# Kernel tuning notes

Hardware: AMD Instinct MI355X
Metric: run time of the kernel (lower is better)

The kernel has to match this reference:

```python
import jax, jax.numpy as jnp
import numpy as np

LN_EPS = 1e-5

def setup_inputs() -> dict:
    key = jax.random.key(0)
    ks = jax.random.split(key, 10)
    N, E, H, V, L, OUT, G = 100000, 600000, 128, 65, 4, 32, 64
    x_tokens = jax.random.randint(ks[0], (N, 2), 0, V, dtype=jnp.int32)
    edge_index = jax.random.randint(ks[1], (2, E), 0, N, dtype=jnp.int32)
    batch = jnp.sort(jax.random.randint(ks[2], (N,), 0, G)).astype(jnp.int64)
    s = 0.05
    key_emb = jax.random.normal(ks[3], (V, H), jnp.float32) * s
    val_emb = jax.random.normal(ks[4], (V, H), jnp.float32) * s
    Ws = jax.random.normal(ks[5], (L, H, H), jnp.float32) * (1.0 / np.sqrt(H))
    bs = jax.random.normal(ks[6], (L, H), jnp.float32) * s
    ln_g = jnp.ones((L, H), jnp.float32)
    ln_b = jnp.zeros((L, H), jnp.float32)
    out_W = jax.random.normal(ks[7], (OUT, H), jnp.float32) * (1.0 / np.sqrt(H))
    return {"x_tokens": x_tokens, "edge_index": edge_index, "batch": batch,
            "key_emb": key_emb, "val_emb": val_emb, "Ws": Ws, "bs": bs,
            "ln_g": ln_g, "ln_b": ln_b, "out_W": out_W}

def _layer_norm(x, g, b):
    mu = jnp.mean(x, axis=-1, keepdims=True)
    var = jnp.mean(jnp.square(x - mu), axis=-1, keepdims=True)
    return (x - mu) * jax.lax.rsqrt(var + LN_EPS) * g + b

def reference(x_tokens, edge_index, batch, key_emb, val_emb, Ws, bs, ln_g, ln_b, out_W):
    N = x_tokens.shape[0]
    L = Ws.shape[0]
    # layer-0: key + value embedding lookup -> [N, H]
    x = key_emb[x_tokens[:, 0]] + val_emb[x_tokens[:, 1]]
    # GCN normalization with self-loops (computed once; edges fixed per layer)
    loop = jnp.arange(N, dtype=edge_index.dtype)
    src = jnp.concatenate([edge_index[0], loop])  # [E+N]
    dst = jnp.concatenate([edge_index[1], loop])
    deg = jax.ops.segment_sum(jnp.ones_like(dst, dtype=x.dtype), dst, num_segments=N)
    dis = jnp.where(deg > 0, jax.lax.rsqrt(jnp.maximum(deg, 1.0)), 0.0)
    norm = (dis[src] * dis[dst])[:, None]  # [E+N, 1]
    for i in range(L):
        xw = x @ Ws[i]  # [N, H]
        agg = jax.ops.segment_sum(norm * xw[src], dst, num_segments=N) + bs[i]
        new_x = jax.nn.relu(agg)          # use_activation
        x = x + new_x                      # use_residual
        x = _layer_norm(x, ln_g[i], ln_b[i])  # use_layer_norm
    logits = x @ out_W.T  # Linear(bias=False) -> [N, out_dim]
    return logits
```

## Files before the change

### kernel.cpp

```cpp
#include <hip/hip_runtime.h>

#define H 128
#define LN_EPS 1e-5f
#define TROW 66

typedef unsigned short u16;
typedef unsigned int u32;
typedef __attribute__((ext_vector_type(8))) short bf16x8;
typedef __attribute__((ext_vector_type(4))) float f32x4;

__device__ __forceinline__ float bflo(u32 u){ return __uint_as_float(u << 16); }
__device__ __forceinline__ float bfhi(u32 u){ return __uint_as_float(u & 0xFFFF0000u); }
__device__ __forceinline__ float bf1(u16 u){ return __uint_as_float(((u32)u) << 16); }
__device__ __forceinline__ u16 f2bu(float f){
  u32 u = __float_as_uint(f);
  return (u16)((u + 0x7FFFu + ((u >> 16) & 1u)) >> 16);
}

__device__ __forceinline__ float ldf(const void* p, int i, bool isbf){
  return isbf ? bf1(reinterpret_cast<const u16*>(p)[i])
              : reinterpret_cast<const float*>(p)[i];
}


__global__ void k_convert(const void* __restrict__ kemb, const void* __restrict__ vemb,
                          const void* __restrict__ Ws,   const void* __restrict__ bs,
                          const void* __restrict__ lng,  const void* __restrict__ lnb,
                          const void* __restrict__ outW,
                          float* __restrict__ kemb_f, float* __restrict__ vemb_f,
                          u16* __restrict__ W_c, float* __restrict__ bs_f,
                          float* __restrict__ lng_f, float* __restrict__ lnb_f,
                          u16* __restrict__ outW_b, int* __restrict__ flag,
                          int V, int L, int OUT){
  bool isbf = (*reinterpret_cast<const u32*>(lng) == 0x3F803F80u);
  if (blockIdx.x == 0 && threadIdx.x == 0) flag[0] = isbf ? 1 : 0;
  int i = blockIdx.x * blockDim.x + threadIdx.x;
  int nEmb = V * H;
  int nW   = L * H * H;
  int nVec = L * H;
  int nOut = OUT * H;
  if (i < nEmb){ kemb_f[i] = ldf(kemb, i, isbf); vemb_f[i] = ldf(vemb, i, isbf); }
  if (i < nW){
    int j = i & 7, lane = (i >> 3) & 63, g = i >> 9;
    int s = g & 3, cg = (g >> 2) & 7, l = g >> 5;
    int k = s * 32 + (lane >> 4) * 8 + j;
    int n = cg * 16 + (lane & 15);
    W_c[i] = f2bu(ldf(Ws, l * H * H + k * H + n, isbf));
  }
  if (i < nVec){ bs_f[i] = ldf(bs, i, isbf); lng_f[i] = ldf(lng, i, isbf);
                 lnb_f[i] = ldf(lnb, i, isbf); }
  if (i < nOut){ outW_b[i] = f2bu(ldf(outW, i, isbf)); }
}


__global__ void k_count(const int* __restrict__ dst, int E, int* __restrict__ deg){
  int i = blockIdx.x * blockDim.x + threadIdx.x;
  if (i < E) atomicAdd(&deg[dst[i]], 1);
}

__device__ __forceinline__ int paddedLen(int d){ return (d + 4) & ~3; }

__global__ void k_bsum(const int* __restrict__ deg, int* __restrict__ bsum, int N){
  __shared__ int sh[256];
  int i = blockIdx.x * 256 + threadIdx.x;
  sh[threadIdx.x] = (i < N) ? paddedLen(deg[i]) : 0;
  __syncthreads();
  for (int off = 128; off > 0; off >>= 1){
    if (threadIdx.x < off) sh[threadIdx.x] += sh[threadIdx.x + off];
    __syncthreads();
  }
  if (threadIdx.x == 0) bsum[blockIdx.x] = sh[0];
}

__global__ void k_bscan(int* __restrict__ bsum, int nb){
  __shared__ int sh[1024];
  int t = threadIdx.x;
  sh[t] = (t < nb) ? bsum[t] : 0;
  __syncthreads();
  for (int off = 1; off < 1024; off <<= 1){
    int add = (t >= off) ? sh[t - off] : 0;
    __syncthreads();
    sh[t] += add;
    __syncthreads();
  }
  if (t < nb) bsum[t] = (t > 0) ? sh[t - 1] : 0;
}

__global__ void k_scan2(const int* __restrict__ deg, const int* __restrict__ bsum,
                        int* __restrict__ row_ptr, float* __restrict__ dis,
                        int* __restrict__ cursor, int2* __restrict__ csr, int N){
  __shared__ int sh[256];
  int i = blockIdx.x * 256 + threadIdx.x;
  int d = (i < N) ? deg[i] : 0;
  int v = (i < N) ? paddedLen(d) : 0;
  sh[threadIdx.x] = v;
  __syncthreads();
  for (int off = 1; off < 256; off <<= 1){
    int add = (threadIdx.x >= off) ? sh[threadIdx.x - off] : 0;
    __syncthreads();
    sh[threadIdx.x] += add;
    __syncthreads();
  }
  int excl = sh[threadIdx.x] - v + bsum[blockIdx.x];
  if (i < N){
    row_ptr[i] = excl;
    float r = rsqrtf((float)(d + 1));
    dis[i] = r;
    cursor[i] = 1;
    csr[excl] = make_int2(i * (H / 2), __float_as_int(r * r));
    for (int p = excl + d + 1; p < excl + v; p++)
      csr[p] = make_int2(0, 0);
  }
  if (i == N - 1) row_ptr[N] = excl + v;
}

__global__ void k_fill(const int* __restrict__ src, const int* __restrict__ dst, int E,
                       const float* __restrict__ dis, const int* __restrict__ row_ptr,
                       int* __restrict__ cursor, int2* __restrict__ csr){
  int i = blockIdx.x * blockDim.x + threadIdx.x;
  if (i >= E) return;
  int s = src[i], d = dst[i];
  int pos = atomicAdd(&cursor[d], 1);
  csr[row_ptr[d] + pos] = make_int2(s * (H / 2), __float_as_int(dis[s] * dis[d]));
}


__global__ __launch_bounds__(256) void k_embed(const int* __restrict__ tok,
                        const float* __restrict__ kemb, const float* __restrict__ vemb,
                        u16* __restrict__ xb, int N){
  int n = blockIdx.x * 4 + (threadIdx.x >> 6);
  if (n >= N) return;
  int h0 = (threadIdx.x & 63) * 2;
  int t0 = tok[n * 2], t1 = tok[n * 2 + 1];
  float2 k2 = *reinterpret_cast<const float2*>(&kemb[t0 * H + h0]);
  float2 v2 = *reinterpret_cast<const float2*>(&vemb[t1 * H + h0]);
  *reinterpret_cast<u32*>(&xb[(size_t)n * H + h0]) =
      (u32)f2bu(k2.x + v2.x) | ((u32)f2bu(k2.y + v2.y) << 16);
}


__global__ __launch_bounds__(256) void k_gemm(const u16* __restrict__ xb,
                                              const u16* __restrict__ Wc,
                                              u16* __restrict__ xw, int npairs){
  int wid = threadIdx.x >> 6, lane = threadIdx.x & 63;
  int sp = wid >> 1;
  int ch = wid & 1;
  int r = lane & 15, kq = lane >> 4;
  bf16x8 wf[4][4];
  #pragma unroll
  for (int c = 0; c < 4; c++)
    #pragma unroll
    for (int s = 0; s < 4; s++)
      wf[c][s] = *reinterpret_cast<const bf16x8*>(
          Wc + (size_t)((((ch * 4 + c) * 4 + s) * 64 + lane) << 3));
  for (int p = blockIdx.x; p < npairs; p += gridDim.x){
    int node0 = (p * 2 + sp) << 4;
    const u16* xrow = xb + (size_t)node0 * H + r * H + kq * 8;
    bf16x8 xf[4];
    #pragma unroll
    for (int s = 0; s < 4; s++)
      xf[s] = *reinterpret_cast<const bf16x8*>(xrow + s * 32);
    f32x4 acc[4] = {{0,0,0,0},{0,0,0,0},{0,0,0,0},{0,0,0,0}};
    #pragma unroll
    for (int s = 0; s < 4; s++)
      #pragma unroll
      for (int c = 0; c < 4; c++)
        acc[c] = __builtin_amdgcn_mfma_f32_16x16x32_bf16(wf[c][s], xf[s], acc[c], 0, 0, 0);
    u16* orow = xw + (size_t)(node0 + r) * H + ch * 64 + kq * 4;
    #pragma unroll
    for (int c = 0; c < 4; c++){
      u32 lo = (u32)f2bu(acc[c][0]) | ((u32)f2bu(acc[c][1]) << 16);
      u32 hi = (u32)f2bu(acc[c][2]) | ((u32)f2bu(acc[c][3]) << 16);
      *reinterpret_cast<uint2*>(orow + c * 16) = make_uint2(lo, hi);
    }
  }
}


__device__ __forceinline__ void gather4(const u32* __restrict__ xw32,
    const int* __restrict__ row_ptr, const int2* __restrict__ csr,
    const float* __restrict__ bias, const float* __restrict__ gamma,
    const float* __restrict__ beta,
    u16* __restrict__ xb, int N, u32* __restrict__ tile, bool writeGlobal){
  int lane = threadIdx.x & 63;
  int w = threadIdx.x >> 6;
  int n0 = blockIdx.x * 16 + 4 * w;
  int h0 = lane * 2;
  const int4* csr4 = reinterpret_cast<const int4*>(csr);
  int rp0 = __builtin_amdgcn_readfirstlane(row_ptr[min(n0, N)]);
  int rp1 = __builtin_amdgcn_readfirstlane(row_ptr[min(n0 + 1, N)]);
  int rp2 = __builtin_amdgcn_readfirstlane(row_ptr[min(n0 + 2, N)]);
  int rp3 = __builtin_amdgcn_readfirstlane(row_ptr[min(n0 + 3, N)]);
  int rp4 = __builtin_amdgcn_readfirstlane(row_ptr[min(n0 + 4, N)]);
  int l0 = rp1 - rp0, l1 = rp2 - rp1, l2 = rp3 - rp2, l3 = rp4 - rp3;
  bool val0 = n0 < N, val1 = n0 + 1 < N, val2 = n0 + 2 < N, val3 = n0 + 3 < N;
  u32 xv0 = val0 ? *reinterpret_cast<const u32*>(&xb[(size_t)n0 * H + h0]) : 0u;
  u32 xv1 = val1 ? *reinterpret_cast<const u32*>(&xb[(size_t)(n0 + 1) * H + h0]) : 0u;
  u32 xv2 = val2 ? *reinterpret_cast<const u32*>(&xb[(size_t)(n0 + 2) * H + h0]) : 0u;
  u32 xv3 = val3 ? *reinterpret_cast<const u32*>(&xb[(size_t)(n0 + 3) * H + h0]) : 0u;
  float2 b2 = *reinterpret_cast<const float2*>(&bias[h0]);
  float2 g2 = *reinterpret_cast<const float2*>(&gamma[h0]);
  float2 t2 = *reinterpret_cast<const float2*>(&beta[h0]);
  float a00 = 0.f, a01 = 0.f, a10 = 0.f, a11 = 0.f;
  float a20 = 0.f, a21 = 0.f, a30 = 0.f, a31 = 0.f;
#define EDGE(CX, CY, A0, A1) { \
    u32 cx = (u32)__builtin_amdgcn_readfirstlane(CX); \
    float wgt = __uint_as_float((u32)__builtin_amdgcn_readfirstlane(CY)); \
    u32 v = xw32[cx + lane]; \
    A0 = fmaf(wgt, bflo(v), A0); A1 = fmaf(wgt, bfhi(v), A1); }
  int c01 = min(l0, l1), c23 = min(l2, l3), c4 = min(c01, c23);
  int i = 0;
  for (; i < c4; i += 4){
    int4 A0 = csr4[(rp0 + i) >> 1], B0 = csr4[((rp0 + i) >> 1) + 1];
    int4 A1 = csr4[(rp1 + i) >> 1], B1 = csr4[((rp1 + i) >> 1) + 1];
    int4 A2 = csr4[(rp2 + i) >> 1], B2 = csr4[((rp2 + i) >> 1) + 1];
    int4 A3 = csr4[(rp3 + i) >> 1], B3 = csr4[((rp3 + i) >> 1) + 1];
    EDGE(A0.x, A0.y, a00, a01) EDGE(A1.x, A1.y, a10, a11)
    EDGE(A2.x, A2.y, a20, a21) EDGE(A3.x, A3.y, a30, a31)
    EDGE(A0.z, A0.w, a00, a01) EDGE(A1.z, A1.w, a10, a11)
    EDGE(A2.z, A2.w, a20, a21) EDGE(A3.z, A3.w, a30, a31)
    EDGE(B0.x, B0.y, a00, a01) EDGE(B1.x, B1.y, a10, a11)
    EDGE(B2.x, B2.y, a20, a21) EDGE(B3.x, B3.y, a30, a31)
    EDGE(B0.z, B0.w, a00, a01) EDGE(B1.z, B1.w, a10, a11)
    EDGE(B2.z, B2.w, a20, a21) EDGE(B3.z, B3.w, a30, a31)
  }
  int j = i;
  for (; j < c01; j += 4){
    int4 A0 = csr4[(rp0 + j) >> 1], B0 = csr4[((rp0 + j) >> 1) + 1];
    int4 A1 = csr4[(rp1 + j) >> 1], B1 = csr4[((rp1 + j) >> 1) + 1];
    EDGE(A0.x, A0.y, a00, a01) EDGE(A1.x, A1.y, a10, a11)
    EDGE(A0.z, A0.w, a00, a01) EDGE(A1.z, A1.w, a10, a11)
    EDGE(B0.x, B0.y, a00, a01) EDGE(B1.x, B1.y, a10, a11)
    EDGE(B0.z, B0.w, a00, a01) EDGE(B1.z, B1.w, a10, a11)
  }
  int j0 = j;
  for (; j0 < l0; j0 += 4){
    int4 A0 = csr4[(rp0 + j0) >> 1], B0 = csr4[((rp0 + j0) >> 1) + 1];
    EDGE(A0.x, A0.y, a00, a01) EDGE(A0.z, A0.w, a00, a01)
    EDGE(B0.x, B0.y, a00, a01) EDGE(B0.z, B0.w, a00, a01)
  }
  int j1 = j;
  for (; j1 < l1; j1 += 4){
    int4 A1 = csr4[(rp1 + j1) >> 1], B1 = csr4[((rp1 + j1) >> 1) + 1];
    EDGE(A1.x, A1.y, a10, a11) EDGE(A1.z, A1.w, a10, a11)
    EDGE(B1.x, B1.y, a10, a11) EDGE(B1.z, B1.w, a10, a11)
  }
  int k = i;
  for (; k < c23; k += 4){
    int4 A2 = csr4[(rp2 + k) >> 1], B2 = csr4[((rp2 + k) >> 1) + 1];
    int4 A3 = csr4[(rp3 + k) >> 1], B3 = csr4[((rp3 + k) >> 1) + 1];
    EDGE(A2.x, A2.y, a20, a21) EDGE(A3.x, A3.y, a30, a31)
    EDGE(A2.z, A2.w, a20, a21) EDGE(A3.z, A3.w, a30, a31)
    EDGE(B2.x, B2.y, a20, a21) EDGE(B3.x, B3.y, a30, a31)
    EDGE(B2.z, B2.w, a20, a21) EDGE(B3.z, B3.w, a30, a31)
  }
  int k2 = k;
  for (; k2 < l2; k2 += 4){
    int4 A2 = csr4[(rp2 + k2) >> 1], B2 = csr4[((rp2 + k2) >> 1) + 1];
    EDGE(A2.x, A2.y, a20, a21) EDGE(A2.z, A2.w, a20, a21)
    EDGE(B2.x, B2.y, a20, a21) EDGE(B2.z, B2.w, a20, a21)
  }
  int k3 = k;
  for (; k3 < l3; k3 += 4){
    int4 A3 = csr4[(rp3 + k3) >> 1], B3 = csr4[((rp3 + k3) >> 1) + 1];
    EDGE(A3.x, A3.y, a30, a31) EDGE(A3.z, A3.w, a30, a31)
    EDGE(B3.x, B3.y, a30, a31) EDGE(B3.z, B3.w, a30, a31)
  }
#undef EDGE
  float v0 = fmaxf(a00 + b2.x, 0.f) + bflo(xv0), v1 = fmaxf(a01 + b2.y, 0.f) + bfhi(xv0);
  float u0 = fmaxf(a10 + b2.x, 0.f) + bflo(xv1), u1 = fmaxf(a11 + b2.y, 0.f) + bfhi(xv1);
  float p0 = fmaxf(a20 + b2.x, 0.f) + bflo(xv2), p1 = fmaxf(a21 + b2.y, 0.f) + bfhi(xv2);
  float r0 = fmaxf(a30 + b2.x, 0.f) + bflo(xv3), r1 = fmaxf(a31 + b2.y, 0.f) + bfhi(xv3);
  float s0 = v0 + v1, s1 = u0 + u1, s2 = p0 + p1, s3 = r0 + r1;
  #pragma unroll
  for (int off = 32; off > 0; off >>= 1){
    s0 += __shfl_xor(s0, off); s1 += __shfl_xor(s1, off);
    s2 += __shfl_xor(s2, off); s3 += __shfl_xor(s3, off);
  }
  float mu0 = s0 * (1.f / 128.f), mu1 = s1 * (1.f / 128.f);
  float mu2 = s2 * (1.f / 128.f), mu3 = s3 * (1.f / 128.f);
  float d00 = v0 - mu0, d01 = v1 - mu0, d10 = u0 - mu1, d11 = u1 - mu1;
  float d20 = p0 - mu2, d21 = p1 - mu2, d30 = r0 - mu3, d31 = r1 - mu3;
  float q0 = d00 * d00 + d01 * d01, q1 = d10 * d10 + d11 * d11;
  float q2 = d20 * d20 + d21 * d21, q3 = d30 * d30 + d31 * d31;
  #pragma unroll
  for (int off = 32; off > 0; off >>= 1){
    q0 += __shfl_xor(q0, off); q1 += __shfl_xor(q1, off);
    q2 += __shfl_xor(q2, off); q3 += __shfl_xor(q3, off);
  }
  float i0 = rsqrtf(q0 * (1.f / 128.f) + LN_EPS), i1 = rsqrtf(q1 * (1.f / 128.f) + LN_EPS);
  float i2 = rsqrtf(q2 * (1.f / 128.f) + LN_EPS), i3 = rsqrtf(q3 * (1.f / 128.f) + LN_EPS);
  u32 w0 = (u32)f2bu(d00 * i0 * g2.x + t2.x) | ((u32)f2bu(d01 * i0 * g2.y + t2.y) << 16);
  u32 w1 = (u32)f2bu(d10 * i1 * g2.x + t2.x) | ((u32)f2bu(d11 * i1 * g2.y + t2.y) << 16);
  u32 w2 = (u32)f2bu(d20 * i2 * g2.x + t2.x) | ((u32)f2bu(d21 * i2 * g2.y + t2.y) << 16);
  u32 w3 = (u32)f2bu(d30 * i3 * g2.x + t2.x) | ((u32)f2bu(d31 * i3 * g2.y + t2.y) << 16);
  tile[(4 * w + 0) * TROW + lane] = val0 ? w0 : 0u;
  tile[(4 * w + 1) * TROW + lane] = val1 ? w1 : 0u;
  tile[(4 * w + 2) * TROW + lane] = val2 ? w2 : 0u;
  tile[(4 * w + 3) * TROW + lane] = val3 ? w3 : 0u;
  if (writeGlobal){
    if (val0) *reinterpret_cast<u32*>(&xb[(size_t)n0 * H + h0]) = w0;
    if (val1) *reinterpret_cast<u32*>(&xb[(size_t)(n0 + 1) * H + h0]) = w1;
    if (val2) *reinterpret_cast<u32*>(&xb[(size_t)(n0 + 2) * H + h0]) = w2;
    if (val3) *reinterpret_cast<u32*>(&xb[(size_t)(n0 + 3) * H + h0]) = w3;
  }
}

__global__ __launch_bounds__(256) void k_fgemm(const u32* __restrict__ xw32,
    const int* __restrict__ row_ptr, const int2* __restrict__ csr,
    const float* __restrict__ bias, const float* __restrict__ gamma,
    const float* __restrict__ beta,
    u16* __restrict__ xb, const u16* __restrict__ Wc,
    u16* __restrict__ xw_out, int N){
  __shared__ u32 tile[16 * TROW];
  int lane = threadIdx.x & 63, w = threadIdx.x >> 6;
  int r = lane & 15, kq = lane >> 4;
  bf16x8 wfr[2][4];
  #pragma unroll
  for (int c = 0; c < 2; c++)
    #pragma unroll
    for (int s = 0; s < 4; s++)
      wfr[c][s] = *reinterpret_cast<const bf16x8*>(
          Wc + (size_t)((((2 * w + c) * 4 + s) * 64 + lane) << 3));
  gather4(xw32, row_ptr, csr, bias, gamma, beta, xb, N, tile, true);
  __syncthreads();
  int node = blockIdx.x * 16 + r;
  if (node >= N) return;
  const u16* t16 = reinterpret_cast<const u16*>(tile);
  f32x4 acc[2] = {{0,0,0,0},{0,0,0,0}};
  #pragma unroll
  for (int s = 0; s < 4; s++){
    bf16x8 xf = *reinterpret_cast<const bf16x8*>(t16 + r * (2 * TROW) + s * 32 + kq * 8);
    #pragma unroll
    for (int c = 0; c < 2; c++)
      acc[c] = __builtin_amdgcn_mfma_f32_16x16x32_bf16(wfr[c][s], xf, acc[c], 0, 0, 0);
  }
  #pragma unroll
  for (int c = 0; c < 2; c++){
    u32 lo = (u32)f2bu(acc[c][0]) | ((u32)f2bu(acc[c][1]) << 16);
    u32 hi = (u32)f2bu(acc[c][2]) | ((u32)f2bu(acc[c][3]) << 16);
    *reinterpret_cast<uint2*>(xw_out + (size_t)node * H + (2 * w + c) * 16 + kq * 4) =
        make_uint2(lo, hi);
  }
}

__global__ __launch_bounds__(256) void k_fout(const u32* __restrict__ xw32,
    const int* __restrict__ row_ptr, const int2* __restrict__ csr,
    const float* __restrict__ bias, const float* __restrict__ gamma,
    const float* __restrict__ beta,
    u16* __restrict__ xb, const u16* __restrict__ oWb,
    u16* __restrict__ out16, float* __restrict__ outf,
    const int* __restrict__ flag, int N){
  __shared__ u32 tile[16 * TROW];
  int lane = threadIdx.x & 63, w = threadIdx.x >> 6;
  int r = lane & 15, kq = lane >> 4;
  bf16x8 wfr[4];
  if (w < 2){
    #pragma unroll
    for (int s = 0; s < 4; s++)
      wfr[s] = *reinterpret_cast<const bf16x8*>(oWb + (w * 16 + r) * H + s * 32 + kq * 8);
  }
  gather4(xw32, row_ptr, csr, bias, gamma, beta, xb, N, tile, false);
  __syncthreads();
  if (w >= 2) return;
  int node = blockIdx.x * 16 + r;
  if (node >= N) return;
  const u16* t16 = reinterpret_cast<const u16*>(tile);
  f32x4 acc = {0.f, 0.f, 0.f, 0.f};
  #pragma unroll
  for (int s = 0; s < 4; s++){
    bf16x8 xf = *reinterpret_cast<const bf16x8*>(t16 + r * (2 * TROW) + s * 32 + kq * 8);
    acc = __builtin_amdgcn_mfma_f32_16x16x32_bf16(wfr[s], xf, acc, 0, 0, 0);
  }
  if (flag[0]){
    u32 lo = (u32)f2bu(acc[0]) | ((u32)f2bu(acc[1]) << 16);
    u32 hi = (u32)f2bu(acc[2]) | ((u32)f2bu(acc[3]) << 16);
    *reinterpret_cast<uint2*>(out16 + (size_t)node * 32 + w * 16 + kq * 4) =
        make_uint2(lo, hi);
  } else {
    *reinterpret_cast<f32x4*>(outf + (size_t)node * 32 + w * 16 + kq * 4) = acc;
  }
}


extern "C" void kernel_launch(void* const* d_in, const int* in_sizes, int n_in,
                              void* d_out, int out_size, void* d_ws, size_t ws_size,
                              hipStream_t stream){
  const int*  x_tokens = (const int*)d_in[0];
  const int*  edge_idx = (const int*)d_in[1];
  const void* kemb = d_in[3];
  const void* vemb = d_in[4];
  const void* Ws   = d_in[5];
  const void* bs   = d_in[6];
  const void* lng  = d_in[7];
  const void* lnb  = d_in[8];
  const void* outW = d_in[9];

  int N   = in_sizes[0] / 2;
  int E   = in_sizes[1] / 2;
  int V   = in_sizes[3] / H;
  int L   = in_sizes[5] / (H * H);
  int OUT = in_sizes[9] / H;

  char* ws = (char*)d_ws;
  size_t off = 0;
  auto alloc = [&](size_t bytes) -> void* {
    void* p = ws + off;
    off += (bytes + 255) & ~(size_t)255;
    return p;
  };
  u16*   xb     = (u16*)  alloc((size_t)N * H * 2);
  u16*   xwA    = (u16*)  alloc((size_t)N * H * 2);
  u16*   xwB    = (u16*)  alloc((size_t)N * H * 2);
  int*   deg    = (int*)  alloc((size_t)N * 4);
  int*   cursor = (int*)  alloc((size_t)N * 4);
  int*   row_ptr= (int*)  alloc((size_t)(N + 1) * 4);
  float* dis    = (float*)alloc((size_t)N * 4);
  int*   bsum   = (int*)  alloc(1024 * 4);
  int2*  csr    = (int2*) alloc(((size_t)E + 4 * (size_t)N) * 8);
  float* kemb_f = (float*)alloc((size_t)V * H * 4);
  float* vemb_f = (float*)alloc((size_t)V * H * 4);
  u16*   W_c    = (u16*)  alloc((size_t)L * H * H * 2);
  float* bs_f   = (float*)alloc((size_t)L * H * 4);
  float* lng_f  = (float*)alloc((size_t)L * H * 4);
  float* lnb_f  = (float*)alloc((size_t)L * H * 4);
  u16*   outW_b = (u16*)  alloc((size_t)OUT * H * 2);
  int*   flag   = (int*)  alloc(256);

  const int* esrc = edge_idx;
  const int* edst = edge_idx + E;

  (void)hipMemsetAsync(deg, 0, (size_t)N * 4, stream);

  int convTotal = L * H * H;
  int cb = (convTotal + 255) / 256;
  k_convert<<<cb, 256, 0, stream>>>(kemb, vemb, Ws, bs, lng, lnb, outW,
                                    kemb_f, vemb_f, W_c, bs_f, lng_f, lnb_f,
                                    outW_b, flag, V, L, OUT);

  int eb = (E + 255) / 256;
  int nb = (N + 255) / 256;
  k_count<<<eb, 256, 0, stream>>>(edst, E, deg);
  k_bsum <<<nb, 256, 0, stream>>>(deg, bsum, N);
  k_bscan<<<1, 1024, 0, stream>>>(bsum, nb);
  k_scan2<<<nb, 256, 0, stream>>>(deg, bsum, row_ptr, dis, cursor, csr, N);
  k_fill <<<eb, 256, 0, stream>>>(esrc, edst, E, dis, row_ptr, cursor, csr);
  k_embed<<<(N + 3) / 4, 256, 0, stream>>>(x_tokens, kemb_f, vemb_f, xb, N);

  int nstrips = (N + 15) / 16;
  int npairs  = (nstrips + 1) / 2;
  k_gemm<<<1024, 256, 0, stream>>>(xb, W_c, xwA, npairs);
  u16* xw_in = xwA; u16* xw_out = xwB;
  for (int l = 0; l < L - 1; l++){
    k_fgemm<<<nstrips, 256, 0, stream>>>((const u32*)xw_in, row_ptr, csr,
                                         bs_f + l * H, lng_f + l * H, lnb_f + l * H,
                                         xb, W_c + (size_t)(l + 1) * H * H,
                                         xw_out, N);
    u16* t = xw_in; xw_in = xw_out; xw_out = t;
  }
  k_fout<<<nstrips, 256, 0, stream>>>((const u32*)xw_in, row_ptr, csr,
                                      bs_f + (L - 1) * H, lng_f + (L - 1) * H,
                                      lnb_f + (L - 1) * H,
                                      xb, outW_b, (u16*)d_out, (float*)d_out,
                                      flag, N);
}
```

Before: 284.5 us.

## Sort nodes by degree so each wave processes similar-length rows

Adds a degree histogram, scan and counting-sort permutation so fused gather/GEMM kernels handle nodes in descending-degree order. Each wave of four nodes then has closely matched edge counts, which cuts the tail loops and divergence where one long row stalls the other three. The cost is three extra small kernels, one more level of indirection per node, and scattered rather than contiguous reads and writes of xb and outputs.

Result: slower. 1.028 ms (+261.4%).

```diff
diff --git a/kernel.cpp b/kernel.cpp
--- a/kernel.cpp
+++ b/kernel.cpp
@@ -125,6 +125,35 @@
 }
 
 
+__global__ void k_hist(const int* __restrict__ deg, int* __restrict__ hist, int N){
+  int i = blockIdx.x * blockDim.x + threadIdx.x;
+  if (i < N) atomicAdd(&hist[min(deg[i], 255)], 1);
+}
+
+__global__ void k_hscan(const int* __restrict__ hist, int* __restrict__ bcur, int N){
+  __shared__ int sh[256];
+  int t = threadIdx.x;
+  sh[t] = hist[t];
+  __syncthreads();
+  for (int off = 1; off < 256; off <<= 1){
+    int add = (t >= off) ? sh[t - off] : 0;
+    __syncthreads();
+    sh[t] += add;
+    __syncthreads();
+  }
+  bcur[t] = N - sh[t];
+}
+
+__global__ void k_perm(const int* __restrict__ deg, int* __restrict__ bcur,
+                       int* __restrict__ perm, int N){
+  int i = blockIdx.x * blockDim.x + threadIdx.x;
+  if (i >= N) return;
+  int b = min(deg[i], 255);
+  int pos = atomicAdd(&bcur[b], 1);
+  perm[pos] = i;
+}
+
+
 __global__ __launch_bounds__(256) void k_embed(const int* __restrict__ tok,
                         const float* __restrict__ kemb, const float* __restrict__ vemb,
                         u16* __restrict__ xb, int N){
@@ -179,6 +208,7 @@
 
 __device__ __forceinline__ void gather4(const u32* __restrict__ xw32,
     const int* __restrict__ row_ptr, const int2* __restrict__ csr,
+    const int* __restrict__ perm,
     const float* __restrict__ bias, const float* __restrict__ gamma,
     const float* __restrict__ beta,
     u16* __restrict__ xb, int N, u32* __restrict__ tile, bool writeGlobal){
@@ -187,17 +217,23 @@
   int n0 = blockIdx.x * 16 + 4 * w;
   int h0 = lane * 2;
   const int4* csr4 = reinterpret_cast<const int4*>(csr);
-  int rp0 = __builtin_amdgcn_readfirstlane(row_ptr[min(n0, N)]);
-  int rp1 = __builtin_amdgcn_readfirstlane(row_ptr[min(n0 + 1, N)]);
-  int rp2 = __builtin_amdgcn_readfirstlane(row_ptr[min(n0 + 2, N)]);
-  int rp3 = __builtin_amdgcn_readfirstlane(row_ptr[min(n0 + 3, N)]);
-  int rp4 = __builtin_amdgcn_readfirstlane(row_ptr[min(n0 + 4, N)]);
-  int l0 = rp1 - rp0, l1 = rp2 - rp1, l2 = rp3 - rp2, l3 = rp4 - rp3;
   bool val0 = n0 < N, val1 = n0 + 1 < N, val2 = n0 + 2 < N, val3 = n0 + 3 < N;
-  u32 xv0 = val0 ? *reinterpret_cast<const u32*>(&xb[(size_t)n0 * H + h0]) : 0u;
-  u32 xv1 = val1 ? *reinterpret_cast<const u32*>(&xb[(size_t)(n0 + 1) * H + h0]) : 0u;
-  u32 xv2 = val2 ? *reinterpret_cast<const u32*>(&xb[(size_t)(n0 + 2) * H + h0]) : 0u;
-  u32 xv3 = val3 ? *reinterpret_cast<const u32*>(&xb[(size_t)(n0 + 3) * H + h0]) : 0u;
+  int p0 = __builtin_amdgcn_readfirstlane(perm[min(n0,     N - 1)]);
+  int p1 = __builtin_amdgcn_readfirstlane(perm[min(n0 + 1, N - 1)]);
+  int p2 = __builtin_amdgcn_readfirstlane(perm[min(n0 + 2, N - 1)]);
+  int p3 = __builtin_amdgcn_readfirstlane(perm[min(n0 + 3, N - 1)]);
+  int rp0 = __builtin_amdgcn_readfirstlane(row_ptr[p0]);
+  int rp1 = __builtin_amdgcn_readfirstlane(row_ptr[p1]);
+  int rp2 = __builtin_amdgcn_readfirstlane(row_ptr[p2]);
+  int rp3 = __builtin_amdgcn_readfirstlane(row_ptr[p3]);
+  int l0 = val0 ? __builtin_amdgcn_readfirstlane(row_ptr[p0 + 1]) - rp0 : 0;
+  int l1 = val1 ? __builtin_amdgcn_readfirstlane(row_ptr[p1 + 1]) - rp1 : 0;
+  int l2 = val2 ? __builtin_amdgcn_readfirstlane(row_ptr[p2 + 1]) - rp2 : 0;
+  int l3 = val3 ? __builtin_amdgcn_readfirstlane(row_ptr[p3 + 1]) - rp3 : 0;
+  u32 xv0 = val0 ? *reinterpret_cast<const u32*>(&xb[(size_t)p0 * H + h0]) : 0u;
+  u32 xv1 = val1 ? *reinterpret_cast<const u32*>(&xb[(size_t)p1 * H + h0]) : 0u;
+  u32 xv2 = val2 ? *reinterpret_cast<const u32*>(&xb[(size_t)p2 * H + h0]) : 0u;
+  u32 xv3 = val3 ? *reinterpret_cast<const u32*>(&xb[(size_t)p3 * H + h0]) : 0u;
   float2 b2 = *reinterpret_cast<const float2*>(&bias[h0]);
   float2 g2 = *reinterpret_cast<const float2*>(&gamma[h0]);
   float2 t2 = *reinterpret_cast<const float2*>(&beta[h0]);
@@ -269,9 +305,9 @@
 #undef EDGE
   float v0 = fmaxf(a00 + b2.x, 0.f) + bflo(xv0), v1 = fmaxf(a01 + b2.y, 0.f) + bfhi(xv0);
   float u0 = fmaxf(a10 + b2.x, 0.f) + bflo(xv1), u1 = fmaxf(a11 + b2.y, 0.f) + bfhi(xv1);
-  float p0 = fmaxf(a20 + b2.x, 0.f) + bflo(xv2), p1 = fmaxf(a21 + b2.y, 0.f) + bfhi(xv2);
+  float p0f = fmaxf(a20 + b2.x, 0.f) + bflo(xv2), p1f = fmaxf(a21 + b2.y, 0.f) + bfhi(xv2);
   float r0 = fmaxf(a30 + b2.x, 0.f) + bflo(xv3), r1 = fmaxf(a31 + b2.y, 0.f) + bfhi(xv3);
-  float s0 = v0 + v1, s1 = u0 + u1, s2 = p0 + p1, s3 = r0 + r1;
+  float s0 = v0 + v1, s1 = u0 + u1, s2 = p0f + p1f, s3 = r0 + r1;
   #pragma unroll
   for (int off = 32; off > 0; off >>= 1){
     s0 += __shfl_xor(s0, off); s1 += __shfl_xor(s1, off);
@@ -280,7 +316,7 @@
   float mu0 = s0 * (1.f / 128.f), mu1 = s1 * (1.f / 128.f);
   float mu2 = s2 * (1.f / 128.f), mu3 = s3 * (1.f / 128.f);
   float d00 = v0 - mu0, d01 = v1 - mu0, d10 = u0 - mu1, d11 = u1 - mu1;
-  float d20 = p0 - mu2, d21 = p1 - mu2, d30 = r0 - mu3, d31 = r1 - mu3;
+  float d20 = p0f - mu2, d21 = p1f - mu2, d30 = r0 - mu3, d31 = r1 - mu3;
   float q0 = d00 * d00 + d01 * d01, q1 = d10 * d10 + d11 * d11;
   float q2 = d20 * d20 + d21 * d21, q3 = d30 * d30 + d31 * d31;
   #pragma unroll
@@ -299,15 +335,16 @@
   tile[(4 * w + 2) * TROW + lane] = val2 ? w2 : 0u;
   tile[(4 * w + 3) * TROW + lane] = val3 ? w3 : 0u;
   if (writeGlobal){
-    if (val0) *reinterpret_cast<u32*>(&xb[(size_t)n0 * H + h0]) = w0;
-    if (val1) *reinterpret_cast<u32*>(&xb[(size_t)(n0 + 1) * H + h0]) = w1;
-    if (val2) *reinterpret_cast<u32*>(&xb[(size_t)(n0 + 2) * H + h0]) = w2;
-    if (val3) *reinterpret_cast<u32*>(&xb[(size_t)(n0 + 3) * H + h0]) = w3;
+    if (val0) *reinterpret_cast<u32*>(&xb[(size_t)p0 * H + h0]) = w0;
+    if (val1) *reinterpret_cast<u32*>(&xb[(size_t)p1 * H + h0]) = w1;
+    if (val2) *reinterpret_cast<u32*>(&xb[(size_t)p2 * H + h0]) = w2;
+    if (val3) *reinterpret_cast<u32*>(&xb[(size_t)p3 * H + h0]) = w3;
   }
 }
 
 __global__ __launch_bounds__(256) void k_fgemm(const u32* __restrict__ xw32,
     const int* __restrict__ row_ptr, const int2* __restrict__ csr,
+    const int* __restrict__ perm,
     const float* __restrict__ bias, const float* __restrict__ gamma,
     const float* __restrict__ beta,
     u16* __restrict__ xb, const u16* __restrict__ Wc,
@@ -322,10 +359,11 @@
     for (int s = 0; s < 4; s++)
       wfr[c][s] = *reinterpret_cast<const bf16x8*>(
           Wc + (size_t)((((2 * w + c) * 4 + s) * 64 + lane) << 3));
-  gather4(xw32, row_ptr, csr, bias, gamma, beta, xb, N, tile, true);
+  gather4(xw32, row_ptr, csr, perm, bias, gamma, beta, xb, N, tile, true);
   __syncthreads();
-  int node = blockIdx.x * 16 + r;
-  if (node >= N) return;
+  int si = blockIdx.x * 16 + r;
+  if (si >= N) return;
+  int node = perm[si];
   const u16* t16 = reinterpret_cast<const u16*>(tile);
   f32x4 acc[2] = {{0,0,0,0},{0,0,0,0}};
   #pragma unroll
@@ -346,6 +384,7 @@
 
 __global__ __launch_bounds__(256) void k_fout(const u32* __restrict__ xw32,
     const int* __restrict__ row_ptr, const int2* __restrict__ csr,
+    const int* __restrict__ perm,
     const float* __restrict__ bias, const float* __restrict__ gamma,
     const float* __restrict__ beta,
     u16* __restrict__ xb, const u16* __restrict__ oWb,
@@ -360,11 +399,12 @@
     for (int s = 0; s < 4; s++)
       wfr[s] = *reinterpret_cast<const bf16x8*>(oWb + (w * 16 + r) * H + s * 32 + kq * 8);
   }
-  gather4(xw32, row_ptr, csr, bias, gamma, beta, xb, N, tile, false);
+  gather4(xw32, row_ptr, csr, perm, bias, gamma, beta, xb, N, tile, false);
   __syncthreads();
   if (w >= 2) return;
-  int node = blockIdx.x * 16 + r;
-  if (node >= N) return;
+  int si = blockIdx.x * 16 + r;
+  if (si >= N) return;
+  int node = perm[si];
   const u16* t16 = reinterpret_cast<const u16*>(tile);
   f32x4 acc = {0.f, 0.f, 0.f, 0.f};
   #pragma unroll
@@ -413,10 +453,13 @@
   u16*   xwA    = (u16*)  alloc((size_t)N * H * 2);
   u16*   xwB    = (u16*)  alloc((size_t)N * H * 2);
   int*   deg    = (int*)  alloc((size_t)N * 4);
+  int*   hist   = (int*)  alloc(256 * 4);
   int*   cursor = (int*)  alloc((size_t)N * 4);
   int*   row_ptr= (int*)  alloc((size_t)(N + 1) * 4);
   float* dis    = (float*)alloc((size_t)N * 4);
   int*   bsum   = (int*)  alloc(1024 * 4);
+  int*   bcur   = (int*)  alloc(256 * 4);
+  int*   perm   = (int*)  alloc((size_t)N * 4);
   int2*  csr    = (int2*) alloc(((size_t)E + 4 * (size_t)N) * 8);
   float* kemb_f = (float*)alloc((size_t)V * H * 4);
   float* vemb_f = (float*)alloc((size_t)V * H * 4);
@@ -431,6 +474,7 @@
   const int* edst = edge_idx + E;
 
   (void)hipMemsetAsync(deg, 0, (size_t)N * 4, stream);
+  (void)hipMemsetAsync(hist, 0, 256 * 4, stream);
 
   int convTotal = L * H * H;
   int cb = (convTotal + 255) / 256;
@@ -441,6 +485,9 @@
   int eb = (E + 255) / 256;
   int nb = (N + 255) / 256;
   k_count<<<eb, 256, 0, stream>>>(edst, E, deg);
+  k_hist <<<nb, 256, 0, stream>>>(deg, hist, N);
+  k_hscan<<<1, 256, 0, stream>>>(hist, bcur, N);
+  k_perm <<<nb, 256, 0, stream>>>(deg, bcur, perm, N);
   k_bsum <<<nb, 256, 0, stream>>>(deg, bsum, N);
   k_bscan<<<1, 1024, 0, stream>>>(bsum, nb);
   k_scan2<<<nb, 256, 0, stream>>>(deg, bsum, row_ptr, dis, cursor, csr, N);
@@ -452,13 +499,13 @@
   k_gemm<<<1024, 256, 0, stream>>>(xb, W_c, xwA, npairs);
   u16* xw_in = xwA; u16* xw_out = xwB;
   for (int l = 0; l < L - 1; l++){
-    k_fgemm<<<nstrips, 256, 0, stream>>>((const u32*)xw_in, row_ptr, csr,
+    k_fgemm<<<nstrips, 256, 0, stream>>>((const u32*)xw_in, row_ptr, csr, perm,
                                          bs_f + l * H, lng_f + l * H, lnb_f + l * H,
                                          xb, W_c + (size_t)(l + 1) * H * H,
                                          xw_out, N);
     u16* t = xw_in; xw_in = xw_out; xw_out = t;
   }
-  k_fout<<<nstrips, 256, 0, stream>>>((const u32*)xw_in, row_ptr, csr,
+  k_fout<<<nstrips, 256, 0, stream>>>((const u32*)xw_in, row_ptr, csr, perm,
                                       bs_f + (L - 1) * H, lng_f + (L - 1) * H,
                                       lnb_f + (L - 1) * H,
                                       xb, outW_b, (u16*)d_out, (float*)d_out,
```
